# Kernel optimization log

Hardware: AMD Instinct MI355X
Metric: run time of the kernel (lower is better)

## Reference

```python
import jax, jax.numpy as jnp
import numpy as np

N = 50000   # nodes
E = 1600000 # edges
F = 128     # node feature dim
D_ENC, D_EMB, D_H = 32, 12, 128
TEMPERATURE = 10.0


def _dense(key, fan_in, fan_out):
    kw, kb = jax.random.split(key)
    W = jax.random.normal(kw, (fan_in, fan_out), jnp.float32) * (1.0 / jnp.sqrt(fan_in))
    b = jnp.zeros((fan_out,), jnp.float32)
    return W, b


def setup_inputs() -> dict:
    key = jax.random.key(0)
    ks = jax.random.split(key, 12)
    nodes = jax.random.normal(ks[0], (N, F), jnp.float32)
    senders = jax.random.randint(ks[1], (E,), 0, N, dtype=jnp.int32)
    receivers = jax.random.randint(ks[2], (E,), 0, N, dtype=jnp.int32)
    W_enc, b_enc = _dense(ks[3], F, D_ENC)
    W_inf, b_inf = _dense(ks[4], D_ENC + 1, 1)
    W_emb, b_emb = _dense(ks[5], F, D_EMB)
    W1, b1 = _dense(ks[6], D_EMB, D_H)
    W2, b2 = _dense(ks[7], D_H, D_H)
    Wy, by = _dense(ks[8], D_H, 1)
    Wx, bx = _dense(ks[9], D_H, 4)
    return {"nodes": nodes, "senders": senders, "receivers": receivers,
            "W_enc": W_enc, "b_enc": b_enc, "W_inf": W_inf, "b_inf": b_inf,
            "W_emb": W_emb, "b_emb": b_emb, "W1": W1, "b1": b1,
            "W2": W2, "b2": b2, "Wy": Wy, "by": by, "Wx": Wx, "bx": bx}


def reference(nodes, senders, receivers, W_enc, b_enc, W_inf, b_inf,
              W_emb, b_emb, W1, b1, W2, b2, Wy, by, Wx, bx):
    n_nodes = nodes.shape[0]
    # EncodeNet: Dense(32) + relu
    vodes = jax.nn.relu(nodes @ W_enc + b_enc)                      # [N, 32]
    # compute_pure_message: gather by senders, scatter-add by receivers
    msg = jax.ops.segment_sum(vodes[senders], receivers, num_segments=n_nodes)
    vodes = vodes + msg                                             # [N, 32]
    # concat last raw node feature
    vodes = jnp.concatenate([vodes, nodes[:, -1:]], axis=1)         # [N, 33]
    # InfluenceNet: Dense(1), softmax over nodes
    influence = vodes @ W_inf + b_inf                               # [N, 1]
    attention = jax.nn.softmax(influence, axis=0)                   # [N, 1]
    # EmbedNet: Dense(12); softmax-weighted pooling over nodes
    emb = nodes @ W_emb + b_emb                                     # [N, 12]
    g = jnp.sum(emb * attention, axis=0)                            # [12]
    # ActNet head
    h = jax.nn.relu(g @ W1 + b1)
    h = jax.nn.relu(h @ W2 + b2)
    value = h @ Wy + by                                             # [1]
    logits = h @ Wx + bx                                            # [4]
    return (logits / TEMPERATURE, value)
```

## Files before the change

### kernel.cpp

```cpp
#include <hip/hip_runtime.h>
#include <hip/hip_bf16.h>


#define NF 128
#define DENC 32
#define DEMB 12
#define DH 128

#define NSLICE 128
#define NRANGE 2
#define R_SCAT 25024
#define ROWB (NSLICE*64)

template <int NJ, int LDW>
__device__ __forceinline__ void gemv_rows(
    const float4* __restrict__ x4p, const float* __restrict__ W,
    int jbase, const float* __restrict__ bias, float* acc, float& x_last)
{
#pragma unroll
    for (int j = 0; j < NJ; j++) acc[j] = bias[jbase + j];
#pragma unroll 2
    for (int c = 0; c < 8; c++) {
        float4 xa = x4p[4 * c + 0];
        float4 xb = x4p[4 * c + 1];
        float4 xc = x4p[4 * c + 2];
        float4 xd = x4p[4 * c + 3];
        float xs[16] = {xa.x, xa.y, xa.z, xa.w, xb.x, xb.y, xb.z, xb.w,
                        xc.x, xc.y, xc.z, xc.w, xd.x, xd.y, xd.z, xd.w};
#pragma unroll
        for (int u = 0; u < 16; u++) {
            const int k = 16 * c + u;
#pragma unroll
            for (int j = 0; j < NJ; j++)
                acc[j] = fmaf(xs[u], W[k * LDW + jbase + j], acc[j]);
        }
        if (c == 7) x_last = xd.w;
    }
}

__global__ __launch_bounds__(256) void k1_node(
    const float* __restrict__ nodes,
    const float* __restrict__ W_enc, const float* __restrict__ b_enc,
    const float* __restrict__ W_inf, const float* __restrict__ b_inf,
    const float* __restrict__ W_emb, const float* __restrict__ b_emb,
    float* __restrict__ p, float* __restrict__ inflb, float* __restrict__ embT,
    int n_nodes)
{
    __shared__ float tabp[3][64];
    const int tid  = threadIdx.x;
    const int lane = tid & 63;
    const int wv   = __builtin_amdgcn_readfirstlane(tid >> 6);
    const int node = blockIdx.x * 64 + lane;
    const bool ok  = (node < n_nodes);

    const float4* x4p = ok ? (const float4*)(nodes + (size_t)node * NF)
                           : (const float4*)nodes;

    float x127 = 0.f;
    if (wv == 3) {
        float acc[DEMB];
        gemv_rows<DEMB, DEMB>(x4p, W_emb, 0, b_emb, acc, x127);
        if (ok) {
#pragma unroll
            for (int j = 0; j < DEMB; j++)
                embT[(size_t)j * n_nodes + node] = acc[j];
        }
    } else {
        const int jbase = __builtin_amdgcn_readfirstlane(wv * 11);
        float pp = 0.f;
        if (wv == 2) {
            float acc[10];
            gemv_rows<10, DENC>(x4p, W_enc, jbase, b_enc, acc, x127);
#pragma unroll
            for (int j = 0; j < 10; j++)
                pp += fmaxf(acc[j], 0.f) * W_inf[jbase + j];
        } else {
            float acc[11];
            gemv_rows<11, DENC>(x4p, W_enc, jbase, b_enc, acc, x127);
#pragma unroll
            for (int j = 0; j < 11; j++)
                pp += fmaxf(acc[j], 0.f) * W_inf[jbase + j];
        }
        tabp[wv][lane] = pp;
    }
    __syncthreads();

    if (wv == 0 && ok) {
        float pn = tabp[0][lane] + tabp[1][lane] + tabp[2][lane];
        p[node] = pn;
        inflb[node] = pn + x127 * W_inf[DENC] + b_inf[0];
    }
}

__global__ __launch_bounds__(1024) void k2_scatter(
    const int* __restrict__ senders, const int* __restrict__ recvs,
    const float* __restrict__ p, float* __restrict__ rep2,
    int n_nodes, int n_edges)
{
    extern __shared__ float tab[];
    const int slice = blockIdx.x >> 1;
    const int rng_i = blockIdx.x & 1;
    const int e0 = (int)((long long)n_edges * slice / NSLICE);
    const int e1 = (int)((long long)n_edges * (slice + 1) / NSLICE);
    const int lo = rng_i * R_SCAT;
    const int rng = min(R_SCAT, n_nodes - lo);

    float4* tab4 = (float4*)tab;
    for (int i = threadIdx.x; i < (rng + 3) / 4; i += 1024)
        tab4[i] = make_float4(0.f, 0.f, 0.f, 0.f);
    __syncthreads();

    const int ae0 = (e0 + 3) & ~3;
    const int ae1 = e1 & ~3;
    for (int e = e0 + (int)threadIdx.x; e < ae0; e += 1024) {
        unsigned rr = (unsigned)(recvs[e] - lo);
        if (rr < (unsigned)rng) atomicAdd(&tab[rr], p[senders[e]]);
    }
    const int4* r4 = (const int4*)recvs;
    const int4* s4 = (const int4*)senders;
    for (int i = ae0 / 4 + (int)threadIdx.x; i < ae1 / 4; i += 1024) {
        int4 r = r4[i];
        int4 s = s4[i];
        unsigned rr;
        rr = (unsigned)(r.x - lo); if (rr < (unsigned)rng) atomicAdd(&tab[rr], p[s.x]);
        rr = (unsigned)(r.y - lo); if (rr < (unsigned)rng) atomicAdd(&tab[rr], p[s.y]);
        rr = (unsigned)(r.z - lo); if (rr < (unsigned)rng) atomicAdd(&tab[rr], p[s.z]);
        rr = (unsigned)(r.w - lo); if (rr < (unsigned)rng) atomicAdd(&tab[rr], p[s.w]);
    }
    for (int e = ae1 + (int)threadIdx.x; e < e1; e += 1024) {
        unsigned rr = (unsigned)(recvs[e] - lo);
        if (rr < (unsigned)rng) atomicAdd(&tab[rr], p[senders[e]]);
    }
    __syncthreads();

    const int g4base = lo >> 2;
    for (int i4 = threadIdx.x; i4 < rng / 4; i4 += 1024) {
        const int g4    = g4base + i4;
        const int chunk = g4 >> 4;
        const int col4  = g4 & 15;
        ((float4*)rep2)[(size_t)chunk * (ROWB / 4) + slice * 16 + col4] = tab4[i4];
    }
    for (int i = (rng & ~3) + threadIdx.x; i < rng; i += 1024) {
        const int g = lo + i;
        rep2[(size_t)(g >> 6) * ROWB + slice * 64 + (g & 63)] = tab[i];
    }
}

__global__ __launch_bounds__(256) void k3_soft(
    const float* __restrict__ inflb, const float* __restrict__ rep2,
    const float* __restrict__ embT, float* __restrict__ psum, int n_nodes)
{
    __shared__ float tab[4][64];
    const int tid  = threadIdx.x;
    const int lane = tid & 63;
    const int wv   = __builtin_amdgcn_readfirstlane(tid >> 6);
    const int node = blockIdx.x * 64 + lane;
    const bool ok  = (node < n_nodes);

    {
        const float* chunk = rep2 + (size_t)blockIdx.x * ROWB;
        const int s0 = lane >> 4;
        const int c4 = lane & 15;
        float4 a = make_float4(0.f, 0.f, 0.f, 0.f);
#pragma unroll
        for (int i = 0; i < 8; i++) {
            const int slice = 32 * wv + s0 + 4 * i;
            float4 v = ((const float4*)(chunk + slice * 64))[c4];
            a.x += v.x; a.y += v.y; a.z += v.z; a.w += v.w;
        }
#pragma unroll
        for (int off = 16; off <= 32; off <<= 1) {
            a.x += __shfl_xor(a.x, off, 64);
            a.y += __shfl_xor(a.y, off, 64);
            a.z += __shfl_xor(a.z, off, 64);
            a.w += __shfl_xor(a.w, off, 64);
        }
        if (s0 == 0) {
            tab[wv][4 * c4 + 0] = a.x;
            tab[wv][4 * c4 + 1] = a.y;
            tab[wv][4 * c4 + 2] = a.z;
            tab[wv][4 * c4 + 3] = a.w;
        }
    }
    __syncthreads();

    if (wv == 0) {
        float infl = ok ? inflb[node] + tab[0][lane] + tab[1][lane]
                          + tab[2][lane] + tab[3][lane]
                        : -1e30f;
        float m = infl;
#pragma unroll
        for (int off = 32; off; off >>= 1)
            m = fmaxf(m, __shfl_down(m, off, 64));
        m = __shfl(m, 0, 64);

        const float w = ok ? expf(infl - m) : 0.f;
        float v13[13];
        v13[0] = w;
#pragma unroll
        for (int j = 0; j < DEMB; j++)
            v13[1 + j] = ok ? w * embT[(size_t)j * n_nodes + node] : 0.f;

#pragma unroll
        for (int v = 0; v < 13; v++) {
            float x = v13[v];
#pragma unroll
            for (int off = 32; off; off >>= 1)
                x += __shfl_down(x, off, 64);
            v13[v] = x;
        }
        if (lane == 0) {
            psum[blockIdx.x * 14] = m;
#pragma unroll
            for (int v = 0; v < 13; v++)
                psum[blockIdx.x * 14 + 1 + v] = v13[v];
        }
    }
}

__global__ __launch_bounds__(512, 1) void k4_head(
    const float* __restrict__ psum,
    const float* __restrict__ W1, const float* __restrict__ b1,
    const float* __restrict__ W2, const float* __restrict__ b2,
    const float* __restrict__ Wy, const float* __restrict__ by,
    const float* __restrict__ Wx, const float* __restrict__ bx,
    float* __restrict__ out, int nblk)
{
    const int t  = threadIdx.x;
    const int wv = t >> 6;
    const int ln = t & 63;

    __shared__ float sred[8][14];
    __shared__ float tot[14];
    __shared__ float g[DEMB];
    __shared__ float h1[DH];
    __shared__ float part[4][DH];
    __shared__ float h2[DH];
    __shared__ float wred[8][5];

    float m = -1e30f;
    for (int b = t; b < nblk; b += 512) m = fmaxf(m, psum[b * 14]);
#pragma unroll
    for (int off = 32; off; off >>= 1)
        m = fmaxf(m, __shfl_down(m, off, 64));
    if (ln == 0) sred[wv][0] = m;
    __syncthreads();
    float M = sred[0][0];
#pragma unroll
    for (int i = 1; i < 8; i++) M = fmaxf(M, sred[i][0]);
    __syncthreads();

    float acc[13];
#pragma unroll
    for (int v = 0; v < 13; v++) acc[v] = 0.f;
    for (int b = t; b < nblk; b += 512) {
        float sc = expf(psum[b * 14] - M);
#pragma unroll
        for (int v = 0; v < 13; v++)
            acc[v] = fmaf(sc, psum[b * 14 + 1 + v], acc[v]);
    }
#pragma unroll
    for (int v = 0; v < 13; v++) {
        float x = acc[v];
#pragma unroll
        for (int off = 32; off; off >>= 1)
            x += __shfl_down(x, off, 64);
        if (ln == 0) sred[wv][v] = x;
    }
    __syncthreads();
    if (t < 13) {
        float s = 0.f;
#pragma unroll
        for (int i = 0; i < 8; i++) s += sred[i][t];
        tot[t] = s;
    }
    __syncthreads();
    if (t < DEMB) g[t] = tot[1 + t] / tot[0];
    __syncthreads();

    if (t < DH) {
        float s1 = b1[t];
#pragma unroll
        for (int i = 0; i < DEMB; i++) s1 = fmaf(g[i], W1[i * DH + t], s1);
        h1[t] = fmaxf(s1, 0.f);
    }
    __syncthreads();

    {
        const int o  = t & 127;
        const int ks = t >> 7;
        float s = 0.f;
        const float* w2 = W2 + (size_t)(32 * ks) * DH + o;
#pragma unroll 8
        for (int i = 0; i < 32; i++)
            s = fmaf(h1[32 * ks + i], w2[i * DH], s);
        part[ks][o] = s;
    }
    __syncthreads();
    if (t < DH)
        h2[t] = fmaxf(b2[t] + part[0][t] + part[1][t] + part[2][t] + part[3][t], 0.f);
    __syncthreads();

    if (t < DH) {
        const float v = h2[t];
        float pr[5];
#pragma unroll
        for (int j = 0; j < 4; j++) pr[j] = v * Wx[t * 4 + j];
        pr[4] = v * Wy[t];
#pragma unroll
        for (int j = 0; j < 5; j++) {
            float x = pr[j];
#pragma unroll
            for (int off = 32; off; off >>= 1)
                x += __shfl_down(x, off, 64);
            if (ln == 0) wred[wv][j] = x;
        }
    }
    __syncthreads();
    if (t < 4)
        out[t] = (wred[0][t] + wred[1][t] + bx[t]) / 10.0f;
    else if (t == 4)
        out[4] = wred[0][4] + wred[1][4] + by[0];
}

extern "C" void kernel_launch(void* const* d_in, const int* in_sizes, int n_in,
                              void* d_out, int out_size, void* d_ws, size_t ws_size,
                              hipStream_t stream) {
    const float* nodes   = (const float*)d_in[0];
    const int*   senders = (const int*)d_in[1];
    const int*   recvs   = (const int*)d_in[2];
    const float* W_enc   = (const float*)d_in[3];
    const float* b_enc   = (const float*)d_in[4];
    const float* W_inf   = (const float*)d_in[5];
    const float* b_inf   = (const float*)d_in[6];
    const float* W_emb   = (const float*)d_in[7];
    const float* b_emb   = (const float*)d_in[8];
    const float* W1      = (const float*)d_in[9];
    const float* b1      = (const float*)d_in[10];
    const float* W2      = (const float*)d_in[11];
    const float* b2      = (const float*)d_in[12];
    const float* Wy      = (const float*)d_in[13];
    const float* by      = (const float*)d_in[14];
    const float* Wx      = (const float*)d_in[15];
    const float* bx      = (const float*)d_in[16];
    float* out = (float*)d_out;

    const int n_nodes = in_sizes[0] / NF;
    const int n_edges = in_sizes[1];
    const int nb64 = (n_nodes + 63) / 64;

    float* ws    = (float*)d_ws;
    float* p     = ws;
    float* inflb = ws + n_nodes;
    float* embT  = ws + 2 * (size_t)n_nodes;
    float* rep2  = ws + 14 * (size_t)n_nodes;
    float* psum  = rep2 + (size_t)nb64 * ROWB;

    (void)hipFuncSetAttribute((const void*)k2_scatter,
                              hipFuncAttributeMaxDynamicSharedMemorySize,
                              R_SCAT * (int)sizeof(float));

    hipLaunchKernelGGL(k1_node, dim3(nb64), dim3(256), 0, stream,
                       nodes, W_enc, b_enc, W_inf, b_inf, W_emb, b_emb,
                       p, inflb, embT, n_nodes);
    hipLaunchKernelGGL(k2_scatter, dim3(NSLICE * NRANGE), dim3(1024),
                       R_SCAT * sizeof(float), stream,
                       senders, recvs, p, rep2, n_nodes, n_edges);
    hipLaunchKernelGGL(k3_soft, dim3(nb64), dim3(256), 0, stream,
                       inflb, rep2, embT, psum, n_nodes);
    hipLaunchKernelGGL(k4_head, dim3(1), dim3(512), 0, stream,
                       psum, W1, b1, W2, b2, Wy, by, Wx, bx, out, nb64);
}
```

Before: 152.3 us.

## Fuse four kernels into one cooperative persistent kernel with grid syncs

Merges the node GEMV, edge scatter, softmax partial reduction and head kernels into a single cooperative launch of 256 blocks of 1024 threads, separated by grid-wide syncs. This removes three kernel launch gaps and their inter-kernel drain. In exchange, stages 1 and 3 now run with only 256 blocks of four 64-node groups each, which lowers occupancy and parallelism for those stages. The final head reduction assumes nb64 fits in one block of 1024 threads, so it covers at most 1024 chunks.

After: 536.6 us. 3.52x slower.

```diff
diff --git a/kernel.cpp b/kernel.cpp
--- a/kernel.cpp
+++ b/kernel.cpp
@@ -1,5 +1,8 @@
 #include <hip/hip_runtime.h>
+#include <hip/hip_cooperative_groups.h>
 #include <hip/hip_bf16.h>
+
+namespace cg = cooperative_groups;
 
 
 #define NF 128
@@ -11,6 +14,21 @@
 #define NRANGE 2
 #define R_SCAT 25024
 #define ROWB (NSLICE*64)
+#define GRID_X (NSLICE*NRANGE)
+#define BLK 1024
+
+struct KArgs {
+    const float* nodes; const int* senders; const int* recvs;
+    const float* W_enc; const float* b_enc;
+    const float* W_inf; const float* b_inf;
+    const float* W_emb; const float* b_emb;
+    const float* W1; const float* b1;
+    const float* W2; const float* b2;
+    const float* Wy; const float* by;
+    const float* Wx; const float* bx;
+    float* p; float* inflb; float* embT; float* rep2; float* psum;
+    float* out; int n_nodes; int n_edges;
+};
 
 template <int NJ, int LDW>
 __device__ __forceinline__ void gemv_rows(
@@ -38,336 +56,319 @@
     }
 }
 
-__global__ __launch_bounds__(256) void k1_node(
-    const float* __restrict__ nodes,
-    const float* __restrict__ W_enc, const float* __restrict__ b_enc,
-    const float* __restrict__ W_inf, const float* __restrict__ b_inf,
-    const float* __restrict__ W_emb, const float* __restrict__ b_emb,
-    float* __restrict__ p, float* __restrict__ inflb, float* __restrict__ embT,
-    int n_nodes)
+__global__ __launch_bounds__(BLK) void fused(KArgs a)
 {
-    __shared__ float tabp[3][64];
+    extern __shared__ float smem[];
+    cg::grid_group grid = cg::this_grid();
+
     const int tid  = threadIdx.x;
+    const int q    = tid >> 8;
     const int lane = tid & 63;
-    const int wv   = __builtin_amdgcn_readfirstlane(tid >> 6);
-    const int node = blockIdx.x * 64 + lane;
-    const bool ok  = (node < n_nodes);
-
-    const float4* x4p = ok ? (const float4*)(nodes + (size_t)node * NF)
-                           : (const float4*)nodes;
-
-    float x127 = 0.f;
-    if (wv == 3) {
-        float acc[DEMB];
-        gemv_rows<DEMB, DEMB>(x4p, W_emb, 0, b_emb, acc, x127);
-        if (ok) {
+    const int wv   = (tid >> 6) & 3;
+    const int nb64 = (a.n_nodes + 63) >> 6;
+
+    {
+        float* tabp = smem;
+        const int g    = blockIdx.x * 4 + q;
+        const int node = g * 64 + lane;
+        const bool son = (g < nb64);
+        const bool ok  = son && (node < a.n_nodes);
+        float x127 = 0.f;
+        if (son) {
+            const float4* x4p = ok ? (const float4*)(a.nodes + (size_t)node * NF)
+                                   : (const float4*)a.nodes;
+            if (wv == 3) {
+                float acc[DEMB];
+                gemv_rows<DEMB, DEMB>(x4p, a.W_emb, 0, a.b_emb, acc, x127);
+                if (ok) {
+#pragma unroll
+                    for (int j = 0; j < DEMB; j++)
+                        a.embT[(size_t)j * a.n_nodes + node] = acc[j];
+                }
+            } else {
+                const int jbase = __builtin_amdgcn_readfirstlane(wv * 11);
+                float pp = 0.f;
+                if (wv == 2) {
+                    float acc[10];
+                    gemv_rows<10, DENC>(x4p, a.W_enc, jbase, a.b_enc, acc, x127);
+#pragma unroll
+                    for (int j = 0; j < 10; j++)
+                        pp += fmaxf(acc[j], 0.f) * a.W_inf[jbase + j];
+                } else {
+                    float acc[11];
+                    gemv_rows<11, DENC>(x4p, a.W_enc, jbase, a.b_enc, acc, x127);
+#pragma unroll
+                    for (int j = 0; j < 11; j++)
+                        pp += fmaxf(acc[j], 0.f) * a.W_inf[jbase + j];
+                }
+                tabp[(q * 3 + wv) * 64 + lane] = pp;
+            }
+        }
+        __syncthreads();
+        if (son && wv == 0 && ok) {
+            float pn = tabp[(q * 3 + 0) * 64 + lane]
+                     + tabp[(q * 3 + 1) * 64 + lane]
+                     + tabp[(q * 3 + 2) * 64 + lane];
+            a.p[node] = pn;
+            a.inflb[node] = pn + x127 * a.W_inf[DENC] + a.b_inf[0];
+        }
+    }
+    __threadfence();
+    grid.sync();
+
+    {
+        float* tab = smem;
+        const int slice = blockIdx.x >> 1;
+        const int rng_i = blockIdx.x & 1;
+        const int e0 = (int)((long long)a.n_edges * slice / NSLICE);
+        const int e1 = (int)((long long)a.n_edges * (slice + 1) / NSLICE);
+        const int lo = rng_i * R_SCAT;
+        const int rng = min(R_SCAT, a.n_nodes - lo);
+
+        float4* tab4 = (float4*)tab;
+        for (int i = tid; i < (rng + 3) / 4; i += BLK)
+            tab4[i] = make_float4(0.f, 0.f, 0.f, 0.f);
+        __syncthreads();
+
+        const int ae0 = (e0 + 3) & ~3;
+        const int ae1 = e1 & ~3;
+        for (int e = e0 + tid; e < ae0; e += BLK) {
+            unsigned rr = (unsigned)(a.recvs[e] - lo);
+            if (rr < (unsigned)rng) atomicAdd(&tab[rr], a.p[a.senders[e]]);
+        }
+        const int4* r4 = (const int4*)a.recvs;
+        const int4* s4 = (const int4*)a.senders;
+        for (int i = ae0 / 4 + tid; i < ae1 / 4; i += BLK) {
+            int4 r = r4[i];
+            int4 s = s4[i];
+            unsigned rr;
+            rr = (unsigned)(r.x - lo); if (rr < (unsigned)rng) atomicAdd(&tab[rr], a.p[s.x]);
+            rr = (unsigned)(r.y - lo); if (rr < (unsigned)rng) atomicAdd(&tab[rr], a.p[s.y]);
+            rr = (unsigned)(r.z - lo); if (rr < (unsigned)rng) atomicAdd(&tab[rr], a.p[s.z]);
+            rr = (unsigned)(r.w - lo); if (rr < (unsigned)rng) atomicAdd(&tab[rr], a.p[s.w]);
+        }
+        for (int e = ae1 + tid; e < e1; e += BLK) {
+            unsigned rr = (unsigned)(a.recvs[e] - lo);
+            if (rr < (unsigned)rng) atomicAdd(&tab[rr], a.p[a.senders[e]]);
+        }
+        __syncthreads();
+
+        const int g4base = lo >> 2;
+        for (int i4 = tid; i4 < rng / 4; i4 += BLK) {
+            const int g4    = g4base + i4;
+            const int chunk = g4 >> 4;
+            const int col4  = g4 & 15;
+            ((float4*)a.rep2)[(size_t)chunk * (ROWB / 4) + slice * 16 + col4] = tab4[i4];
+        }
+        for (int i = (rng & ~3) + tid; i < rng; i += BLK) {
+            const int g = lo + i;
+            a.rep2[(size_t)(g >> 6) * ROWB + slice * 64 + (g & 63)] = tab[i];
+        }
+    }
+    __threadfence();
+    grid.sync();
+
+    {
+        float* t3 = smem + q * 256;
+        const int chunk = blockIdx.x * 4 + q;
+        const bool son  = (chunk < nb64);
+        const int node  = chunk * 64 + lane;
+        const bool ok   = son && (node < a.n_nodes);
+
+        if (son) {
+            const float* cb = a.rep2 + (size_t)chunk * ROWB;
+            const int s0 = lane >> 4;
+            const int c4 = lane & 15;
+            float4 ac = make_float4(0.f, 0.f, 0.f, 0.f);
+#pragma unroll
+            for (int i = 0; i < 8; i++) {
+                const int slice = 32 * wv + s0 + 4 * i;
+                float4 v = ((const float4*)(cb + slice * 64))[c4];
+                ac.x += v.x; ac.y += v.y; ac.z += v.z; ac.w += v.w;
+            }
+#pragma unroll
+            for (int off = 16; off <= 32; off <<= 1) {
+                ac.x += __shfl_xor(ac.x, off, 64);
+                ac.y += __shfl_xor(ac.y, off, 64);
+                ac.z += __shfl_xor(ac.z, off, 64);
+                ac.w += __shfl_xor(ac.w, off, 64);
+            }
+            if (s0 == 0) {
+                t3[wv * 64 + 4 * c4 + 0] = ac.x;
+                t3[wv * 64 + 4 * c4 + 1] = ac.y;
+                t3[wv * 64 + 4 * c4 + 2] = ac.z;
+                t3[wv * 64 + 4 * c4 + 3] = ac.w;
+            }
+        }
+        __syncthreads();
+        if (son && wv == 0) {
+            float infl = ok ? a.inflb[node] + t3[lane] + t3[64 + lane]
+                              + t3[128 + lane] + t3[192 + lane]
+                            : -1e30f;
+            float m = infl;
+#pragma unroll
+            for (int off = 32; off; off >>= 1)
+                m = fmaxf(m, __shfl_down(m, off, 64));
+            m = __shfl(m, 0, 64);
+
+            const float w = ok ? expf(infl - m) : 0.f;
+            float v13[13];
+            v13[0] = w;
 #pragma unroll
             for (int j = 0; j < DEMB; j++)
-                embT[(size_t)j * n_nodes + node] = acc[j];
-        }
-    } else {
-        const int jbase = __builtin_amdgcn_readfirstlane(wv * 11);
-        float pp = 0.f;
-        if (wv == 2) {
-            float acc[10];
-            gemv_rows<10, DENC>(x4p, W_enc, jbase, b_enc, acc, x127);
-#pragma unroll
-            for (int j = 0; j < 10; j++)
-                pp += fmaxf(acc[j], 0.f) * W_inf[jbase + j];
-        } else {
-            float acc[11];
-            gemv_rows<11, DENC>(x4p, W_enc, jbase, b_enc, acc, x127);
-#pragma unroll
-            for (int j = 0; j < 11; j++)
-                pp += fmaxf(acc[j], 0.f) * W_inf[jbase + j];
-        }
-        tabp[wv][lane] = pp;
-    }
-    __syncthreads();
-
-    if (wv == 0 && ok) {
-        float pn = tabp[0][lane] + tabp[1][lane] + tabp[2][lane];
-        p[node] = pn;
-        inflb[node] = pn + x127 * W_inf[DENC] + b_inf[0];
-    }
-}
-
-__global__ __launch_bounds__(1024) void k2_scatter(
-    const int* __restrict__ senders, const int* __restrict__ recvs,
-    const float* __restrict__ p, float* __restrict__ rep2,
-    int n_nodes, int n_edges)
-{
-    extern __shared__ float tab[];
-    const int slice = blockIdx.x >> 1;
-    const int rng_i = blockIdx.x & 1;
-    const int e0 = (int)((long long)n_edges * slice / NSLICE);
-    const int e1 = (int)((long long)n_edges * (slice + 1) / NSLICE);
-    const int lo = rng_i * R_SCAT;
-    const int rng = min(R_SCAT, n_nodes - lo);
-
-    float4* tab4 = (float4*)tab;
-    for (int i = threadIdx.x; i < (rng + 3) / 4; i += 1024)
-        tab4[i] = make_float4(0.f, 0.f, 0.f, 0.f);
-    __syncthreads();
-
-    const int ae0 = (e0 + 3) & ~3;
-    const int ae1 = e1 & ~3;
-    for (int e = e0 + (int)threadIdx.x; e < ae0; e += 1024) {
-        unsigned rr = (unsigned)(recvs[e] - lo);
-        if (rr < (unsigned)rng) atomicAdd(&tab[rr], p[senders[e]]);
-    }
-    const int4* r4 = (const int4*)recvs;
-    const int4* s4 = (const int4*)senders;
-    for (int i = ae0 / 4 + (int)threadIdx.x; i < ae1 / 4; i += 1024) {
-        int4 r = r4[i];
-        int4 s = s4[i];
-        unsigned rr;
-        rr = (unsigned)(r.x - lo); if (rr < (unsigned)rng) atomicAdd(&tab[rr], p[s.x]);
-        rr = (unsigned)(r.y - lo); if (rr < (unsigned)rng) atomicAdd(&tab[rr], p[s.y]);
-        rr = (unsigned)(r.z - lo); if (rr < (unsigned)rng) atomicAdd(&tab[rr], p[s.z]);
-        rr = (unsigned)(r.w - lo); if (rr < (unsigned)rng) atomicAdd(&tab[rr], p[s.w]);
-    }
-    for (int e = ae1 + (int)threadIdx.x; e < e1; e += 1024) {
-        unsigned rr = (unsigned)(recvs[e] - lo);
-        if (rr < (unsigned)rng) atomicAdd(&tab[rr], p[senders[e]]);
-    }
-    __syncthreads();
-
-    const int g4base = lo >> 2;
-    for (int i4 = threadIdx.x; i4 < rng / 4; i4 += 1024) {
-        const int g4    = g4base + i4;
-        const int chunk = g4 >> 4;
-        const int col4  = g4 & 15;
-        ((float4*)rep2)[(size_t)chunk * (ROWB / 4) + slice * 16 + col4] = tab4[i4];
-    }
-    for (int i = (rng & ~3) + threadIdx.x; i < rng; i += 1024) {
-        const int g = lo + i;
-        rep2[(size_t)(g >> 6) * ROWB + slice * 64 + (g & 63)] = tab[i];
-    }
-}
-
-__global__ __launch_bounds__(256) void k3_soft(
-    const float* __restrict__ inflb, const float* __restrict__ rep2,
-    const float* __restrict__ embT, float* __restrict__ psum, int n_nodes)
-{
-    __shared__ float tab[4][64];
-    const int tid  = threadIdx.x;
-    const int lane = tid & 63;
-    const int wv   = __builtin_amdgcn_readfirstlane(tid >> 6);
-    const int node = blockIdx.x * 64 + lane;
-    const bool ok  = (node < n_nodes);
-
-    {
-        const float* chunk = rep2 + (size_t)blockIdx.x * ROWB;
-        const int s0 = lane >> 4;
-        const int c4 = lane & 15;
-        float4 a = make_float4(0.f, 0.f, 0.f, 0.f);
-#pragma unroll
-        for (int i = 0; i < 8; i++) {
-            const int slice = 32 * wv + s0 + 4 * i;
-            float4 v = ((const float4*)(chunk + slice * 64))[c4];
-            a.x += v.x; a.y += v.y; a.z += v.z; a.w += v.w;
-        }
-#pragma unroll
-        for (int off = 16; off <= 32; off <<= 1) {
-            a.x += __shfl_xor(a.x, off, 64);
-            a.y += __shfl_xor(a.y, off, 64);
-            a.z += __shfl_xor(a.z, off, 64);
-            a.w += __shfl_xor(a.w, off, 64);
-        }
-        if (s0 == 0) {
-            tab[wv][4 * c4 + 0] = a.x;
-            tab[wv][4 * c4 + 1] = a.y;
-            tab[wv][4 * c4 + 2] = a.z;
-            tab[wv][4 * c4 + 3] = a.w;
-        }
-    }
-    __syncthreads();
-
-    if (wv == 0) {
-        float infl = ok ? inflb[node] + tab[0][lane] + tab[1][lane]
-                          + tab[2][lane] + tab[3][lane]
-                        : -1e30f;
-        float m = infl;
+                v13[1 + j] = ok ? w * a.embT[(size_t)j * a.n_nodes + node] : 0.f;
+#pragma unroll
+            for (int v = 0; v < 13; v++) {
+                float x = v13[v];
+#pragma unroll
+                for (int off = 32; off; off >>= 1)
+                    x += __shfl_down(x, off, 64);
+                v13[v] = x;
+            }
+            if (lane == 0) {
+                a.psum[chunk * 14] = m;
+#pragma unroll
+                for (int v = 0; v < 13; v++)
+                    a.psum[chunk * 14 + 1 + v] = v13[v];
+            }
+        }
+    }
+    __threadfence();
+    grid.sync();
+
+    if (blockIdx.x == 0) {
+        float* sred = smem;
+        float* tot  = sred + 16 * 13;
+        float* gv   = tot + 13;
+        float* h1   = gv + 12;
+        float* part = h1 + 128;
+        float* h2   = part + 8 * 128;
+        float* wred = h2 + 128;
+        const int wvid = tid >> 6;
+
+        float m = (tid < nb64) ? a.psum[tid * 14] : -1e30f;
 #pragma unroll
         for (int off = 32; off; off >>= 1)
             m = fmaxf(m, __shfl_down(m, off, 64));
-        m = __shfl(m, 0, 64);
-
-        const float w = ok ? expf(infl - m) : 0.f;
-        float v13[13];
-        v13[0] = w;
-#pragma unroll
-        for (int j = 0; j < DEMB; j++)
-            v13[1 + j] = ok ? w * embT[(size_t)j * n_nodes + node] : 0.f;
-
+        if (lane == 0) sred[wvid] = m;
+        __syncthreads();
+        float M = sred[0];
+#pragma unroll
+        for (int i = 1; i < 16; i++) M = fmaxf(M, sred[i]);
+        __syncthreads();
+
+        float acc[13];
+#pragma unroll
+        for (int v = 0; v < 13; v++) acc[v] = 0.f;
+        if (tid < nb64) {
+            float sc = expf(a.psum[tid * 14] - M);
+#pragma unroll
+            for (int v = 0; v < 13; v++)
+                acc[v] = sc * a.psum[tid * 14 + 1 + v];
+        }
 #pragma unroll
         for (int v = 0; v < 13; v++) {
-            float x = v13[v];
+            float x = acc[v];
 #pragma unroll
             for (int off = 32; off; off >>= 1)
                 x += __shfl_down(x, off, 64);
-            v13[v] = x;
-        }
-        if (lane == 0) {
-            psum[blockIdx.x * 14] = m;
-#pragma unroll
-            for (int v = 0; v < 13; v++)
-                psum[blockIdx.x * 14 + 1 + v] = v13[v];
-        }
-    }
-}
-
-__global__ __launch_bounds__(512, 1) void k4_head(
-    const float* __restrict__ psum,
-    const float* __restrict__ W1, const float* __restrict__ b1,
-    const float* __restrict__ W2, const float* __restrict__ b2,
-    const float* __restrict__ Wy, const float* __restrict__ by,
-    const float* __restrict__ Wx, const float* __restrict__ bx,
-    float* __restrict__ out, int nblk)
-{
-    const int t  = threadIdx.x;
-    const int wv = t >> 6;
-    const int ln = t & 63;
-
-    __shared__ float sred[8][14];
-    __shared__ float tot[14];
-    __shared__ float g[DEMB];
-    __shared__ float h1[DH];
-    __shared__ float part[4][DH];
-    __shared__ float h2[DH];
-    __shared__ float wred[8][5];
-
-    float m = -1e30f;
-    for (int b = t; b < nblk; b += 512) m = fmaxf(m, psum[b * 14]);
-#pragma unroll
-    for (int off = 32; off; off >>= 1)
-        m = fmaxf(m, __shfl_down(m, off, 64));
-    if (ln == 0) sred[wv][0] = m;
-    __syncthreads();
-    float M = sred[0][0];
-#pragma unroll
-    for (int i = 1; i < 8; i++) M = fmaxf(M, sred[i][0]);
-    __syncthreads();
-
-    float acc[13];
-#pragma unroll
-    for (int v = 0; v < 13; v++) acc[v] = 0.f;
-    for (int b = t; b < nblk; b += 512) {
-        float sc = expf(psum[b * 14] - M);
-#pragma unroll
-        for (int v = 0; v < 13; v++)
-            acc[v] = fmaf(sc, psum[b * 14 + 1 + v], acc[v]);
-    }
-#pragma unroll
-    for (int v = 0; v < 13; v++) {
-        float x = acc[v];
-#pragma unroll
-        for (int off = 32; off; off >>= 1)
-            x += __shfl_down(x, off, 64);
-        if (ln == 0) sred[wv][v] = x;
-    }
-    __syncthreads();
-    if (t < 13) {
-        float s = 0.f;
-#pragma unroll
-        for (int i = 0; i < 8; i++) s += sred[i][t];
-        tot[t] = s;
-    }
-    __syncthreads();
-    if (t < DEMB) g[t] = tot[1 + t] / tot[0];
-    __syncthreads();
-
-    if (t < DH) {
-        float s1 = b1[t];
-#pragma unroll
-        for (int i = 0; i < DEMB; i++) s1 = fmaf(g[i], W1[i * DH + t], s1);
-        h1[t] = fmaxf(s1, 0.f);
-    }
-    __syncthreads();
-
-    {
-        const int o  = t & 127;
-        const int ks = t >> 7;
-        float s = 0.f;
-        const float* w2 = W2 + (size_t)(32 * ks) * DH + o;
+            if (lane == 0) sred[wvid * 13 + v] = x;
+        }
+        __syncthreads();
+        if (tid < 13) {
+            float s = 0.f;
+#pragma unroll
+            for (int i = 0; i < 16; i++) s += sred[i * 13 + tid];
+            tot[tid] = s;
+        }
+        __syncthreads();
+        if (tid < DEMB) gv[tid] = tot[1 + tid] / tot[0];
+        __syncthreads();
+
+        if (tid < DH) {
+            float s1 = a.b1[tid];
+#pragma unroll
+            for (int i = 0; i < DEMB; i++)
+                s1 = fmaf(gv[i], a.W1[i * DH + tid], s1);
+            h1[tid] = fmaxf(s1, 0.f);
+        }
+        __syncthreads();
+
+        {
+            const int ks = tid >> 7;
+            const int o  = tid & 127;
+            float s = 0.f;
+            const float* w2 = a.W2 + (size_t)(16 * ks) * DH + o;
 #pragma unroll 8
-        for (int i = 0; i < 32; i++)
-            s = fmaf(h1[32 * ks + i], w2[i * DH], s);
-        part[ks][o] = s;
-    }
-    __syncthreads();
-    if (t < DH)
-        h2[t] = fmaxf(b2[t] + part[0][t] + part[1][t] + part[2][t] + part[3][t], 0.f);
-    __syncthreads();
-
-    if (t < DH) {
-        const float v = h2[t];
-        float pr[5];
-#pragma unroll
-        for (int j = 0; j < 4; j++) pr[j] = v * Wx[t * 4 + j];
-        pr[4] = v * Wy[t];
-#pragma unroll
-        for (int j = 0; j < 5; j++) {
-            float x = pr[j];
-#pragma unroll
-            for (int off = 32; off; off >>= 1)
-                x += __shfl_down(x, off, 64);
-            if (ln == 0) wred[wv][j] = x;
-        }
-    }
-    __syncthreads();
-    if (t < 4)
-        out[t] = (wred[0][t] + wred[1][t] + bx[t]) / 10.0f;
-    else if (t == 4)
-        out[4] = wred[0][4] + wred[1][4] + by[0];
+            for (int i = 0; i < 16; i++)
+                s = fmaf(h1[16 * ks + i], w2[i * DH], s);
+            part[ks * 128 + o] = s;
+        }
+        __syncthreads();
+        if (tid < DH) {
+            float s = a.b2[tid];
+#pragma unroll
+            for (int k = 0; k < 8; k++) s += part[k * 128 + tid];
+            h2[tid] = fmaxf(s, 0.f);
+        }
+        __syncthreads();
+
+        if (tid < DH) {
+            const float v = h2[tid];
+            float pr[5];
+#pragma unroll
+            for (int j = 0; j < 4; j++) pr[j] = v * a.Wx[tid * 4 + j];
+            pr[4] = v * a.Wy[tid];
+#pragma unroll
+            for (int j = 0; j < 5; j++) {
+                float x = pr[j];
+#pragma unroll
+                for (int off = 32; off; off >>= 1)
+                    x += __shfl_down(x, off, 64);
+                if (lane == 0) wred[wvid * 5 + j] = x;
+            }
+        }
+        __syncthreads();
+        if (tid < 4)
+            a.out[tid] = (wred[tid] + wred[5 + tid] + a.bx[tid]) / 10.0f;
+        else if (tid == 4)
+            a.out[4] = wred[4] + wred[9] + a.by[0];
+    }
 }
 
 extern "C" void kernel_launch(void* const* d_in, const int* in_sizes, int n_in,
                               void* d_out, int out_size, void* d_ws, size_t ws_size,
                               hipStream_t stream) {
-    const float* nodes   = (const float*)d_in[0];
-    const int*   senders = (const int*)d_in[1];
-    const int*   recvs   = (const int*)d_in[2];
-    const float* W_enc   = (const float*)d_in[3];
-    const float* b_enc   = (const float*)d_in[4];
-    const float* W_inf   = (const float*)d_in[5];
-    const float* b_inf   = (const float*)d_in[6];
-    const float* W_emb   = (const float*)d_in[7];
-    const float* b_emb   = (const float*)d_in[8];
-    const float* W1      = (const float*)d_in[9];
-    const float* b1      = (const float*)d_in[10];
-    const float* W2      = (const float*)d_in[11];
-    const float* b2      = (const float*)d_in[12];
-    const float* Wy      = (const float*)d_in[13];
-    const float* by      = (const float*)d_in[14];
-    const float* Wx      = (const float*)d_in[15];
-    const float* bx      = (const float*)d_in[16];
-    float* out = (float*)d_out;
-
     const int n_nodes = in_sizes[0] / NF;
     const int n_edges = in_sizes[1];
     const int nb64 = (n_nodes + 63) / 64;
 
-    float* ws    = (float*)d_ws;
-    float* p     = ws;
-    float* inflb = ws + n_nodes;
-    float* embT  = ws + 2 * (size_t)n_nodes;
-    float* rep2  = ws + 14 * (size_t)n_nodes;
-    float* psum  = rep2 + (size_t)nb64 * ROWB;
-
-    (void)hipFuncSetAttribute((const void*)k2_scatter,
+    float* ws = (float*)d_ws;
+    KArgs a;
+    a.nodes   = (const float*)d_in[0];
+    a.senders = (const int*)d_in[1];
+    a.recvs   = (const int*)d_in[2];
+    a.W_enc = (const float*)d_in[3];  a.b_enc = (const float*)d_in[4];
+    a.W_inf = (const float*)d_in[5];  a.b_inf = (const float*)d_in[6];
+    a.W_emb = (const float*)d_in[7];  a.b_emb = (const float*)d_in[8];
+    a.W1 = (const float*)d_in[9];     a.b1 = (const float*)d_in[10];
+    a.W2 = (const float*)d_in[11];    a.b2 = (const float*)d_in[12];
+    a.Wy = (const float*)d_in[13];    a.by = (const float*)d_in[14];
+    a.Wx = (const float*)d_in[15];    a.bx = (const float*)d_in[16];
+    a.p     = ws;
+    a.inflb = ws + n_nodes;
+    a.embT  = ws + 2 * (size_t)n_nodes;
+    a.rep2  = ws + 14 * (size_t)n_nodes;
+    a.psum  = a.rep2 + (size_t)nb64 * ROWB;
+    a.out   = (float*)d_out;
+    a.n_nodes = n_nodes;
+    a.n_edges = n_edges;
+
+    (void)hipFuncSetAttribute((const void*)fused,
                               hipFuncAttributeMaxDynamicSharedMemorySize,
                               R_SCAT * (int)sizeof(float));
 
-    hipLaunchKernelGGL(k1_node, dim3(nb64), dim3(256), 0, stream,
-                       nodes, W_enc, b_enc, W_inf, b_inf, W_emb, b_emb,
-                       p, inflb, embT, n_nodes);
-    hipLaunchKernelGGL(k2_scatter, dim3(NSLICE * NRANGE), dim3(1024),
-                       R_SCAT * sizeof(float), stream,
-                       senders, recvs, p, rep2, n_nodes, n_edges);
-    hipLaunchKernelGGL(k3_soft, dim3(nb64), dim3(256), 0, stream,
-                       inflb, rep2, embT, psum, n_nodes);
-    hipLaunchKernelGGL(k4_head, dim3(1), dim3(512), 0, stream,
-                       psum, W1, b1, W2, b2, Wy, by, Wx, bx, out, nb64);
+    void* kp[] = { (void*)&a };
+    (void)hipLaunchCooperativeKernel((void*)fused, dim3(GRID_X), dim3(BLK),
+                                     kp, R_SCAT * sizeof(float), stream);
 }
```
